# Optimization experiments

Hardware: AMD Instinct MI355X
Metric: run time of the kernel (lower is better)

Reference implementation:

```python
import jax, jax.numpy as jnp
import numpy as np

T, B, I, H, C, O = 4096, 8, 256, 512, 1024, 512
SCHEDULE = 1.0
UPPER_T = 0.3
NIND = int((1.0 - SCHEDULE) * (C - 2) * UPPER_T) + 1  # = 1 (argmax WTA)


def setup_inputs() -> dict:
    key = jax.random.key(0)
    ks = jax.random.split(key, 8)
    def lin(k, fan_out, fan_in):
        s = 1.0 / np.sqrt(fan_in)
        kw, kb = jax.random.split(k)
        return (jax.random.uniform(kw, (fan_out, fan_in), jnp.float32, -s, s),
                jax.random.uniform(kb, (fan_out,), jnp.float32, -s, s))
    i2m_w, i2m_b = lin(ks[0], H, I)
    m2h_w, m2h_b = lin(ks[1], C, H)
    h2o_w, h2o_b = lin(ks[2], O, C)
    return {
        "x": jax.random.normal(ks[3], (T, B, I), jnp.float32),
        "hidden1": jnp.zeros((1,), jnp.float32),  # unused dummy (overwritten in torch forward)
        "i2m_w": i2m_w, "i2m_b": i2m_b,
        "m2h_w": m2h_w, "m2h_b": m2h_b,
        "h2o_w": h2o_w, "h2o_b": h2o_b,
    }


def reference(x, hidden1, i2m_w, i2m_b, m2h_w, m2h_b, h2o_w, h2o_b):
    # linear -> relu
    h = jax.nn.relu(jnp.einsum('tbi,hi->tbh', x, i2m_w) + i2m_b)
    # linear -> relu -> concept pre-activations [T,B,C]
    c = jax.nn.relu(jnp.einsum('tbh,ch->tbc', h, m2h_w) + m2h_b)
    # winner-take-all: top-Nind scatter mask (replaces CPU argsort round-trip)
    _, idx = jax.lax.top_k(c, NIND)  # [T,B,NIND]
    t_ix = jnp.arange(c.shape[0])[:, None, None]
    b_ix = jnp.arange(c.shape[1])[None, :, None]
    mask = jnp.zeros_like(c).at[t_ix, b_ix, idx].set(1.0)
    m = c * mask
    # L2 normalize over concept axis
    m = m / jnp.linalg.norm(m, axis=-1, keepdims=True)
    out = jnp.einsum('tbc,oc->tbo', m, h2o_w) + h2o_b
    return jax.nn.log_softmax(out, axis=-1)
```

## Files before the change

kernel.cpp:

```cpp
#include <hip/hip_runtime.h>
#include <stdint.h>

#define M_ROWS 32768
#define I_DIM 256
#define H_DIM 512
#define C_DIM 1024
#define O_DIM 512

typedef __attribute__((ext_vector_type(8))) short bf16x8;
typedef __attribute__((ext_vector_type(4))) float f32x4;

__device__ __forceinline__ ushort bf16_rne(float f) {
    unsigned u = __float_as_uint(f);
    unsigned r = u + 0x7FFFu + ((u >> 16) & 1u);
    return (ushort)(r >> 16);
}
__device__ __forceinline__ float bf16_f32(ushort h) {
    return __uint_as_float(((unsigned)h) << 16);
}
__device__ __forceinline__ void split2(float f, ushort& hi, ushort& mid) {
    hi = bf16_rne(f);
    mid = bf16_rne(f - bf16_f32(hi));
}

__device__ __forceinline__ void async_ld16(const void* g, void* l) {
    __builtin_amdgcn_global_load_lds(
        (const __attribute__((address_space(1))) void*)g,
        (__attribute__((address_space(3))) void*)l, 16, 0, 0);
}

__device__ __forceinline__ unsigned long long packvi(float v, int col) {
    unsigned u = __float_as_uint(v);
    u = (u & 0x80000000u) ? ~u : (u | 0x80000000u);
    return ((unsigned long long)u << 32) | (unsigned)(~col);
}

__device__ __forceinline__ int slot_of(int kc, int row) {
    return (kc + ((row >> 1) & 3)) & 3;
}

__global__ __launch_bounds__(256)
void prep(const float* __restrict__ W1, ushort* __restrict__ w1h, ushort* __restrict__ w1m,
          const float* __restrict__ W2, ushort* __restrict__ w2h, ushort* __restrict__ w2m,
          const float* __restrict__ Wo, const float* __restrict__ bo,
          float* __restrict__ LS, unsigned long long* __restrict__ part) {
    __shared__ float sred[4];
    const int b = blockIdx.x;
    const int t = threadIdx.x;
    if (b < 320) {
        const int isW1 = (b < 64);
        const float* W = isW1 ? W1 : W2;
        ushort* hh = isW1 ? w1h : w2h;
        ushort* mm = isW1 ? w1m : w2m;
        const int K = isW1 ? I_DIM : H_DIM;
        const int cpr = K >> 3;
        int gid = (isW1 ? b : b - 64) * 256 + t;
        int row = gid / cpr;
        int rem = gid - row * cpr;
        int g = rem >> 2, kc = rem & 3;
        float4 v0 = *(const float4*)(W + (size_t)gid * 8);
        float4 v1 = *(const float4*)(W + (size_t)gid * 8 + 4);
        __align__(16) ushort h[8], m[8];
        float f[8];
        *(float4*)&f[0] = v0; *(float4*)&f[4] = v1;
        #pragma unroll
        for (int j = 0; j < 8; ++j) split2(f[j], h[j], m[j]);
        size_t dst = (size_t)row * K + g * 32 + slot_of(kc, row) * 8;
        *(uint4*)(hh + dst) = *(uint4*)h;
        *(uint4*)(mm + dst) = *(uint4*)m;
    } else if (b < 1344) {
        const int j = b - 320;
        float l0 = Wo[(size_t)t * C_DIM + j] + bo[t];
        float l1 = Wo[(size_t)(t + 256) * C_DIM + j] + bo[t + 256];

        float mx = fmaxf(l0, l1);
        #pragma unroll
        for (int off = 1; off < 64; off <<= 1)
            mx = fmaxf(mx, __shfl_xor(mx, off, 64));
        if ((t & 63) == 0) sred[t >> 6] = mx;
        __syncthreads();
        mx = fmaxf(fmaxf(sred[0], sred[1]), fmaxf(sred[2], sred[3]));
        __syncthreads();

        float s = expf(l0 - mx) + expf(l1 - mx);
        #pragma unroll
        for (int off = 1; off < 64; off <<= 1)
            s += __shfl_xor(s, off, 64);
        if ((t & 63) == 0) sred[t >> 6] = s;
        __syncthreads();
        s = sred[0] + sred[1] + sred[2] + sred[3];

        float lse = mx + logf(s);
        LS[(size_t)j * O_DIM + t] = l0 - lse;
        LS[(size_t)j * O_DIM + t + 256] = l1 - lse;
    } else {
        part[(b - 1344) * 256 + t] = 0ull;
    }
}

__global__ __launch_bounds__(512, 2)
void gemm1_mfma(const float* __restrict__ X, const ushort* __restrict__ W1h,
                const ushort* __restrict__ W1m, const float* __restrict__ b1,
                ushort* __restrict__ Hh, ushort* __restrict__ Hm) {
    __shared__ __align__(16) ushort SMEM[65536];

    const int tid = threadIdx.x;
    const int lane = tid & 63, wave = tid >> 6;
    const int wm = wave >> 2, wn = wave & 3;
    const int lcol = lane & 15, quad = lane >> 4;
    const int lrow = lane >> 2, lk = (lane & 3) * 8;

    const int d = blockIdx.x;
    const int q = d >> 3;
    const int mT = ((d & 7) << 4) + (q >> 1);
    const int nT = q & 1;
    const int mBase = mT * 256;
    const int nBase = nT * 256;

    const int s_row = tid >> 1, s_half = tid & 1;
    const int sl0 = slot_of(s_half * 2,     s_row);
    const int sl1 = slot_of(s_half * 2 + 1, s_row);
    const float* xrow = X + (size_t)(mBase + s_row) * I_DIM + s_half * 16;

    const int bplane = wave >> 2;
    const int brow0 = (wave & 3) * 64;
    const ushort* wp = bplane ? W1m : W1h;
    const ushort* gks = wp + (size_t)(nBase + brow0 + lrow) * I_DIM + lk;

    f32x4 acc[8][4];
    #pragma unroll
    for (int i = 0; i < 8; ++i)
        #pragma unroll
        for (int j = 0; j < 4; ++j)
            acc[i][j] = (f32x4){0.f, 0.f, 0.f, 0.f};

    int aoff[8], boff[4];
    #pragma unroll
    for (int t = 0; t < 8; ++t) {
        int ra = wm * 128 + t * 16 + lcol;
        aoff[t] = ra * 32 + slot_of(quad, ra) * 8;
    }
    #pragma unroll
    for (int t = 0; t < 4; ++t) {
        int rb = wn * 64 + t * 16 + lcol;
        boff[t] = rb * 32 + slot_of(quad, rb) * 8;
    }

    auto loadX = [&](float* f, int k0) {
        const float* ap = xrow + k0;
        *(float4*)&f[0]  = ((const float4*)ap)[0];
        *(float4*)&f[4]  = ((const float4*)ap)[1];
        *(float4*)&f[8]  = ((const float4*)ap)[2];
        *(float4*)&f[12] = ((const float4*)ap)[3];
    };
    auto stageB = [&](int buf, int k0) {
        ushort* bb = SMEM + 32768 + buf * 16384 + bplane * 8192 + brow0 * 32;
        #pragma unroll
        for (int j = 0; j < 4; ++j)
            async_ld16(gks + k0 + (size_t)(j * 16) * I_DIM, bb + j * 512);
    };
    auto writeA = [&](int buf, const float* f) {
        ushort* a0 = SMEM + buf * 16384;
        ushort* a1 = a0 + 8192;
        bf16x8 h0, h1, m0, m1;
        #pragma unroll
        for (int j = 0; j < 8; ++j) {
            ushort hu, mu;
            split2(f[j], hu, mu);
            h0[j] = (short)hu; m0[j] = (short)mu;
            split2(f[j + 8], hu, mu);
            h1[j] = (short)hu; m1[j] = (short)mu;
        }
        *(bf16x8*)&a0[s_row * 32 + sl0 * 8] = h0;
        *(bf16x8*)&a0[s_row * 32 + sl1 * 8] = h1;
        *(bf16x8*)&a1[s_row * 32 + sl0 * 8] = m0;
        *(bf16x8*)&a1[s_row * 32 + sl1 * 8] = m1;
    };

    {
        float fx[16];
        loadX(fx, 0);
        stageB(0, 0);
        writeA(0, fx);
    }
    asm volatile("s_waitcnt lgkmcnt(0)" ::: "memory");
    asm volatile("s_waitcnt vmcnt(0)" ::: "memory");
    __builtin_amdgcn_s_barrier();
    __builtin_amdgcn_sched_barrier(0);

    const int NK = I_DIM / 32;
    #pragma unroll 2
    for (int ks = 0; ks < NK; ++ks) {
        const int cur = ks & 1;
        const bool more = (ks + 1 < NK);
        const ushort* Ac0 = SMEM + cur * 16384;
        const ushort* Ac1 = Ac0 + 8192;
        const ushort* Bc0 = SMEM + 32768 + cur * 16384;
        const ushort* Bc1 = Bc0 + 8192;

        float fn[16];
        if (more) {
            loadX(fn, (ks + 1) * 32);
            stageB(cur ^ 1, (ks + 1) * 32);
            __builtin_amdgcn_sched_barrier(0);
        }

        bf16x8 bh[4], bm[4];
        #pragma unroll
        for (int nt = 0; nt < 4; ++nt) {
            bh[nt] = *(const bf16x8*)&Bc0[boff[nt]];
            bm[nt] = *(const bf16x8*)&Bc1[boff[nt]];
        }
        #pragma unroll
        for (int half = 0; half < 2; ++half) {
            bf16x8 ah[4], am[4];
            #pragma unroll
            for (int mt = 0; mt < 4; ++mt) {
                ah[mt] = *(const bf16x8*)&Ac0[aoff[half * 4 + mt]];
                am[mt] = *(const bf16x8*)&Ac1[aoff[half * 4 + mt]];
            }
            __builtin_amdgcn_s_setprio(1);
            #pragma unroll
            for (int nt = 0; nt < 4; ++nt) {
                #pragma unroll
                for (int mt = 0; mt < 4; ++mt) {
                    f32x4 a = acc[half * 4 + mt][nt];
                    a = __builtin_amdgcn_mfma_f32_16x16x32_bf16(am[mt], bh[nt], a, 0, 0, 0);
                    a = __builtin_amdgcn_mfma_f32_16x16x32_bf16(ah[mt], bm[nt], a, 0, 0, 0);
                    a = __builtin_amdgcn_mfma_f32_16x16x32_bf16(ah[mt], bh[nt], a, 0, 0, 0);
                    acc[half * 4 + mt][nt] = a;
                }
            }
            __builtin_amdgcn_s_setprio(0);
        }

        if (more) writeA(cur ^ 1, fn);
        asm volatile("s_waitcnt lgkmcnt(0)" ::: "memory");
        if (more)
            asm volatile("s_waitcnt vmcnt(0)" ::: "memory");
        __builtin_amdgcn_s_barrier();
        __builtin_amdgcn_sched_barrier(0);
    }

    #pragma unroll
    for (int plane = 0; plane < 2; ++plane) {
        __syncthreads();
        #pragma unroll
        for (int nt = 0; nt < 4; ++nt) {
            int colRel = wn * 64 + nt * 16 + lcol;
            int g = colRel >> 5, kc = (colRel >> 3) & 3, pos = colRel & 7;
            float bias = b1[nBase + colRel];
            #pragma unroll
            for (int mt = 0; mt < 8; ++mt) {
                #pragma unroll
                for (int r = 0; r < 4; ++r) {
                    int rowRel = wm * 128 + mt * 16 + quad * 4 + r;
                    float v = fmaxf(acc[mt][nt][r] + bias, 0.f);
                    ushort hu, mu;
                    split2(v, hu, mu);
                    SMEM[rowRel * 256 + g * 32 + slot_of(kc, rowRel) * 8 + pos]
                        = plane ? mu : hu;
                }
            }
        }
        __syncthreads();
        ushort* dstp = plane ? Hm : Hh;
        #pragma unroll
        for (int l2 = 0; l2 < 16; ++l2) {
            int c = l2 * 512 + tid;
            int row = c >> 5, idx = c & 31;
            *(uint4*)(dstp + (size_t)(mBase + row) * H_DIM + nBase + idx * 8)
                = *(const uint4*)&SMEM[row * 256 + idx * 8];
        }
    }
}

__global__ __launch_bounds__(512, 2)
void gemm2_mfma(const ushort* __restrict__ Hh, const ushort* __restrict__ Hm,
                const ushort* __restrict__ W2h, const ushort* __restrict__ W2m,
                const float* __restrict__ b2,
                unsigned long long* __restrict__ part) {
    __shared__ __align__(16) ushort As[2][2][8192];
    __shared__ __align__(16) ushort Bs[2][2][8192];
    const int tid = threadIdx.x;
    const int lane = tid & 63, wave = tid >> 6;
    const int wm = wave >> 2, wn = wave & 3;
    const int lcol = lane & 15, quad = lane >> 4;
    const int lrow = lane >> 2, lk = (lane & 3) * 8;

    const int d = blockIdx.x;
    const int l = d >> 3;
    const int mT = ((d & 7) << 4) + (l >> 2);
    const int nT = l & 3;
    const int mBase = mT * 256;
    const int nBase = nT * 256;

    const int m_id = wave >> 1;
    const int shalf = wave & 1;
    const ushort* gsrc;
    ushort* l0;
    ushort* l1;
    switch (m_id) {
        case 0:  gsrc = Hh  + (size_t)mBase * H_DIM; l0 = &As[0][0][0]; l1 = &As[1][0][0]; break;
        case 1:  gsrc = Hm  + (size_t)mBase * H_DIM; l0 = &As[0][1][0]; l1 = &As[1][1][0]; break;
        case 2:  gsrc = W2h + (size_t)nBase * H_DIM; l0 = &Bs[0][0][0]; l1 = &Bs[1][0][0]; break;
        default: gsrc = W2m + (size_t)nBase * H_DIM; l0 = &Bs[0][1][0]; l1 = &Bs[1][1][0]; break;
    }
    l0 += shalf * 4096;
    l1 += shalf * 4096;
    const ushort* gks = gsrc + (size_t)(shalf * 128 + lrow) * H_DIM + lk;

    f32x4 acc[8][4];
    #pragma unroll
    for (int i = 0; i < 8; ++i)
        #pragma unroll
        for (int j = 0; j < 4; ++j)
            acc[i][j] = (f32x4){0.f, 0.f, 0.f, 0.f};

    int aoff[8], boff[4];
    #pragma unroll
    for (int t = 0; t < 8; ++t) {
        int ra = wm * 128 + t * 16 + lcol;
        aoff[t] = ra * 32 + slot_of(quad, ra) * 8;
    }
    #pragma unroll
    for (int t = 0; t < 4; ++t) {
        int rb = wn * 64 + t * 16 + lcol;
        boff[t] = rb * 32 + slot_of(quad, rb) * 8;
    }

    auto stage = [&](ushort* lb, int k0) {
        #pragma unroll
        for (int j = 0; j < 8; ++j)
            async_ld16(gks + k0 + (size_t)(j * 16) * H_DIM, lb + j * 512);
    };

    stage(l0, 0);
    asm volatile("s_waitcnt vmcnt(0)" ::: "memory");
    __builtin_amdgcn_s_barrier();
    __builtin_amdgcn_sched_barrier(0);

    const int NK = H_DIM / 32;
    #pragma unroll 2
    for (int ks = 0; ks < NK; ++ks) {
        const int cur = ks & 1;
        if (ks < NK - 1) {
            stage(cur ? l0 : l1, (ks + 1) * 32);
            __builtin_amdgcn_sched_barrier(0);
        }

        bf16x8 bh[4], bm[4];
        #pragma unroll
        for (int nt = 0; nt < 4; ++nt) {
            bh[nt] = *(const bf16x8*)&Bs[cur][0][boff[nt]];
            bm[nt] = *(const bf16x8*)&Bs[cur][1][boff[nt]];
        }
        #pragma unroll
        for (int half = 0; half < 2; ++half) {
            bf16x8 ah[4], am[4];
            #pragma unroll
            for (int mt = 0; mt < 4; ++mt) {
                ah[mt] = *(const bf16x8*)&As[cur][0][aoff[half * 4 + mt]];
                am[mt] = *(const bf16x8*)&As[cur][1][aoff[half * 4 + mt]];
            }
            __builtin_amdgcn_s_setprio(1);
            #pragma unroll
            for (int nt = 0; nt < 4; ++nt) {
                #pragma unroll
                for (int mt = 0; mt < 4; ++mt) {
                    f32x4 a = acc[half * 4 + mt][nt];
                    a = __builtin_amdgcn_mfma_f32_16x16x32_bf16(am[mt], bh[nt], a, 0, 0, 0);
                    a = __builtin_amdgcn_mfma_f32_16x16x32_bf16(ah[mt], bm[nt], a, 0, 0, 0);
                    a = __builtin_amdgcn_mfma_f32_16x16x32_bf16(ah[mt], bh[nt], a, 0, 0, 0);
                    acc[half * 4 + mt][nt] = a;
                }
            }
            __builtin_amdgcn_s_setprio(0);
        }

        if (ks < NK - 1)
            asm volatile("s_waitcnt vmcnt(0)" ::: "memory");
        __builtin_amdgcn_s_barrier();
        __builtin_amdgcn_sched_barrier(0);
    }

    float bias[4];
    #pragma unroll
    for (int nt = 0; nt < 4; ++nt)
        bias[nt] = b2[nBase + wn * 64 + nt * 16 + lcol];

    #pragma unroll
    for (int mt = 0; mt < 8; ++mt) {
        #pragma unroll
        for (int r = 0; r < 4; ++r) {
            unsigned long long best = 0ull;
            #pragma unroll
            for (int nt = 0; nt < 4; ++nt) {
                int col = nBase + wn * 64 + nt * 16 + lcol;
                float v = acc[mt][nt][r] + bias[nt];
                unsigned long long p = packvi(v, col);
                if (p > best) best = p;
            }
            #pragma unroll
            for (int off = 1; off < 16; off <<= 1) {
                unsigned long long o = __shfl_xor((long long)best, off, 64);
                if (o > best) best = o;
            }
            if (lcol == 0) {
                int row = mBase + wm * 128 + mt * 16 + quad * 4 + r;
                atomicMax(&part[row], best);
            }
        }
    }
}

__global__ __launch_bounds__(256)
void gather_out(const unsigned long long* __restrict__ part,
                const float* __restrict__ LS, float* __restrict__ out) {
    __shared__ int js[8];
    const int tid = threadIdx.x;
    const int rbase = blockIdx.x * 8;
    if (tid < 8) {
        unsigned long long best = part[rbase + tid];
        unsigned u = (unsigned)(best >> 32);
        float v = (u & 0x80000000u) ? __uint_as_float(u ^ 0x80000000u)
                                    : __uint_as_float(~u);
        int col = (int)(~(unsigned)best) & (C_DIM - 1);
        js[tid] = (v > 0.f) ? col : 0;
    }
    __syncthreads();
    const float4* LS4 = (const float4*)LS;
    float4* out4 = (float4*)out + (size_t)rbase * 128;
    #pragma unroll
    for (int i = 0; i < 4; ++i) {
        int idx = i * 256 + tid;
        int row = idx >> 7, q = idx & 127;
        out4[idx] = LS4[(size_t)js[row] * 128 + q];
    }
}

extern "C" void kernel_launch(void* const* d_in, const int* in_sizes, int n_in,
                              void* d_out, int out_size, void* d_ws, size_t ws_size,
                              hipStream_t stream) {
    const float* x     = (const float*)d_in[0];
    const float* i2m_w = (const float*)d_in[2];
    const float* i2m_b = (const float*)d_in[3];
    const float* m2h_w = (const float*)d_in[4];
    const float* m2h_b = (const float*)d_in[5];
    const float* h2o_w = (const float*)d_in[6];
    const float* h2o_b = (const float*)d_in[7];
    float* out = (float*)d_out;

    char* ws = (char*)d_ws;
    ushort* w1h = (ushort*)(ws);
    ushort* w1m = (ushort*)(ws + 262144);
    ushort* w2h = (ushort*)(ws + 524288);
    ushort* w2m = (ushort*)(ws + 1572864);
    float*  LS  = (float*)(ws + 2621440);
    unsigned long long* part = (unsigned long long*)(ws + 4718592);

    ushort* Hh = (ushort*)d_out;
    ushort* Hm = Hh + (size_t)M_ROWS * H_DIM;

    prep<<<1472, 256, 0, stream>>>(i2m_w, w1h, w1m, m2h_w, w2h, w2m,
                                   h2o_w, h2o_b, LS, part);
    gemm1_mfma<<<(M_ROWS / 256) * (H_DIM / 256), 512, 0, stream>>>(
        x, w1h, w1m, i2m_b, Hh, Hm);
    gemm2_mfma<<<(M_ROWS / 256) * (C_DIM / 256), 512, 0, stream>>>(
        Hh, Hm, w2h, w2m, m2h_b, part);
    gather_out<<<M_ROWS / 8, 256, 0, stream>>>(part, LS, out);
}
```

Before: 240.3 us.

## Fuse all four stages into one persistent kernel with grid barriers

Replaces the prep, gemm1, gemm2 and gather launches with a single 256-block persistent kernel. The stages are separated by software grid barriers built on global atomic counters. This removes the per-launch overhead and the idle tails between kernels. In exchange it relies on all 256 blocks being co-resident, and a timeout guard in the spin loop could let a block pass the barrier early. Gemm2 now runs its 512 tiles over 256 blocks, and each block handles a larger gather chunk.

Result: slower. 307.8 us (+28.1%).

```diff
diff --git a/kernel.cpp b/kernel.cpp
--- a/kernel.cpp
+++ b/kernel.cpp
@@ -10,6 +10,8 @@
 typedef __attribute__((ext_vector_type(8))) short bf16x8;
 typedef __attribute__((ext_vector_type(4))) float f32x4;
 
+__device__ unsigned g_bar[4] = {0u, 0u, 0u, 0u};
+
 __device__ __forceinline__ ushort bf16_rne(float f) {
     unsigned u = __float_as_uint(f);
     unsigned r = u + 0x7FFFu + ((u >> 16) & 1u);
@@ -39,403 +41,427 @@
     return (kc + ((row >> 1) & 3)) & 3;
 }
 
-__global__ __launch_bounds__(256)
-void prep(const float* __restrict__ W1, ushort* __restrict__ w1h, ushort* __restrict__ w1m,
-          const float* __restrict__ W2, ushort* __restrict__ w2h, ushort* __restrict__ w2m,
-          const float* __restrict__ Wo, const float* __restrict__ bo,
-          float* __restrict__ LS, unsigned long long* __restrict__ part) {
-    __shared__ float sred[4];
+__device__ __forceinline__ void grid_sync(int s) {
+    __syncthreads();
+    if (threadIdx.x == 0) {
+        __threadfence();
+        unsigned old = atomicAdd(&g_bar[s], 1u);
+        unsigned target = (old & ~255u) + 256u;
+        unsigned long long guard = 0ull;
+        while (atomicAdd(&g_bar[s], 0u) < target) {
+            __builtin_amdgcn_s_sleep(2);
+            if (++guard > 10000000ull) break;
+        }
+        __threadfence();
+    }
+    __syncthreads();
+}
+
+__global__ __launch_bounds__(512, 2)
+void mega(const float* X, const float* W1, const float* b1,
+          const float* W2, const float* b2,
+          const float* Wo, const float* bo,
+          ushort* __restrict__ w1h, ushort* __restrict__ w1m,
+          ushort* __restrict__ w2h, ushort* __restrict__ w2m,
+          float* __restrict__ LS, unsigned long long* __restrict__ part,
+          ushort* Hh, ushort* Hm, float* out) {
+    __shared__ __align__(16) ushort SMEM[65536];
+
+    const int tid = threadIdx.x;
     const int b = blockIdx.x;
-    const int t = threadIdx.x;
-    if (b < 320) {
-        const int isW1 = (b < 64);
-        const float* W = isW1 ? W1 : W2;
-        ushort* hh = isW1 ? w1h : w2h;
-        ushort* mm = isW1 ? w1m : w2m;
-        const int K = isW1 ? I_DIM : H_DIM;
-        const int cpr = K >> 3;
-        int gid = (isW1 ? b : b - 64) * 256 + t;
-        int row = gid / cpr;
-        int rem = gid - row * cpr;
-        int g = rem >> 2, kc = rem & 3;
-        float4 v0 = *(const float4*)(W + (size_t)gid * 8);
-        float4 v1 = *(const float4*)(W + (size_t)gid * 8 + 4);
-        __align__(16) ushort h[8], m[8];
-        float f[8];
-        *(float4*)&f[0] = v0; *(float4*)&f[4] = v1;
-        #pragma unroll
-        for (int j = 0; j < 8; ++j) split2(f[j], h[j], m[j]);
-        size_t dst = (size_t)row * K + g * 32 + slot_of(kc, row) * 8;
-        *(uint4*)(hh + dst) = *(uint4*)h;
-        *(uint4*)(mm + dst) = *(uint4*)m;
-    } else if (b < 1344) {
-        const int j = b - 320;
-        float l0 = Wo[(size_t)t * C_DIM + j] + bo[t];
-        float l1 = Wo[(size_t)(t + 256) * C_DIM + j] + bo[t + 256];
-
-        float mx = fmaxf(l0, l1);
-        #pragma unroll
-        for (int off = 1; off < 64; off <<= 1)
-            mx = fmaxf(mx, __shfl_xor(mx, off, 64));
-        if ((t & 63) == 0) sred[t >> 6] = mx;
-        __syncthreads();
-        mx = fmaxf(fmaxf(sred[0], sred[1]), fmaxf(sred[2], sred[3]));
-        __syncthreads();
-
-        float s = expf(l0 - mx) + expf(l1 - mx);
-        #pragma unroll
-        for (int off = 1; off < 64; off <<= 1)
-            s += __shfl_xor(s, off, 64);
-        if ((t & 63) == 0) sred[t >> 6] = s;
-        __syncthreads();
-        s = sred[0] + sred[1] + sred[2] + sred[3];
-
-        float lse = mx + logf(s);
-        LS[(size_t)j * O_DIM + t] = l0 - lse;
-        LS[(size_t)j * O_DIM + t + 256] = l1 - lse;
-    } else {
-        part[(b - 1344) * 256 + t] = 0ull;
-    }
-}
-
-__global__ __launch_bounds__(512, 2)
-void gemm1_mfma(const float* __restrict__ X, const ushort* __restrict__ W1h,
-                const ushort* __restrict__ W1m, const float* __restrict__ b1,
-                ushort* __restrict__ Hh, ushort* __restrict__ Hm) {
-    __shared__ __align__(16) ushort SMEM[65536];
-
-    const int tid = threadIdx.x;
     const int lane = tid & 63, wave = tid >> 6;
     const int wm = wave >> 2, wn = wave & 3;
     const int lcol = lane & 15, quad = lane >> 4;
     const int lrow = lane >> 2, lk = (lane & 3) * 8;
 
-    const int d = blockIdx.x;
-    const int q = d >> 3;
-    const int mT = ((d & 7) << 4) + (q >> 1);
-    const int nT = q & 1;
-    const int mBase = mT * 256;
-    const int nBase = nT * 256;
-
-    const int s_row = tid >> 1, s_half = tid & 1;
-    const int sl0 = slot_of(s_half * 2,     s_row);
-    const int sl1 = slot_of(s_half * 2 + 1, s_row);
-    const float* xrow = X + (size_t)(mBase + s_row) * I_DIM + s_half * 16;
-
-    const int bplane = wave >> 2;
-    const int brow0 = (wave & 3) * 64;
-    const ushort* wp = bplane ? W1m : W1h;
-    const ushort* gks = wp + (size_t)(nBase + brow0 + lrow) * I_DIM + lk;
-
-    f32x4 acc[8][4];
-    #pragma unroll
-    for (int i = 0; i < 8; ++i)
-        #pragma unroll
-        for (int j = 0; j < 4; ++j)
-            acc[i][j] = (f32x4){0.f, 0.f, 0.f, 0.f};
-
-    int aoff[8], boff[4];
-    #pragma unroll
-    for (int t = 0; t < 8; ++t) {
-        int ra = wm * 128 + t * 16 + lcol;
-        aoff[t] = ra * 32 + slot_of(quad, ra) * 8;
+    {
+        int gid = b * 512 + tid;
+        if (gid < 81920) {
+            const int isW1 = (gid < 16384);
+            const float* W = isW1 ? W1 : W2;
+            ushort* hh = isW1 ? w1h : w2h;
+            ushort* mm = isW1 ? w1m : w2m;
+            const int K = isW1 ? I_DIM : H_DIM;
+            const int cpr = K >> 3;
+            int cid = isW1 ? gid : gid - 16384;
+            int row = cid / cpr;
+            int rem = cid - row * cpr;
+            int g = rem >> 2, kc = rem & 3;
+            float4 v0 = *(const float4*)(W + (size_t)cid * 8);
+            float4 v1 = *(const float4*)(W + (size_t)cid * 8 + 4);
+            __align__(16) ushort h[8], m[8];
+            float f[8];
+            *(float4*)&f[0] = v0; *(float4*)&f[4] = v1;
+            #pragma unroll
+            for (int j = 0; j < 8; ++j) split2(f[j], h[j], m[j]);
+            size_t dst = (size_t)row * K + g * 32 + slot_of(kc, row) * 8;
+            *(uint4*)(hh + dst) = *(uint4*)h;
+            *(uint4*)(mm + dst) = *(uint4*)m;
+        }
+        if (gid < 32768) part[gid] = 0ull;
+        float* sred = (float*)SMEM;
+        #pragma unroll 1
+        for (int jj = 0; jj < 4; ++jj) {
+            const int j = b * 4 + jj;
+            float l0 = 0.f, l1 = 0.f, mx = 0.f;
+            if (tid < 256) {
+                l0 = Wo[(size_t)tid * C_DIM + j] + bo[tid];
+                l1 = Wo[(size_t)(tid + 256) * C_DIM + j] + bo[tid + 256];
+                mx = fmaxf(l0, l1);
+                #pragma unroll
+                for (int off = 1; off < 64; off <<= 1)
+                    mx = fmaxf(mx, __shfl_xor(mx, off, 64));
+                if ((tid & 63) == 0) sred[tid >> 6] = mx;
+            }
+            __syncthreads();
+            mx = fmaxf(fmaxf(sred[0], sred[1]), fmaxf(sred[2], sred[3]));
+            __syncthreads();
+            float s = 0.f;
+            if (tid < 256) {
+                s = expf(l0 - mx) + expf(l1 - mx);
+                #pragma unroll
+                for (int off = 1; off < 64; off <<= 1)
+                    s += __shfl_xor(s, off, 64);
+                if ((tid & 63) == 0) sred[tid >> 6] = s;
+            }
+            __syncthreads();
+            s = sred[0] + sred[1] + sred[2] + sred[3];
+            if (tid < 256) {
+                float lse = mx + logf(s);
+                LS[(size_t)j * O_DIM + tid] = l0 - lse;
+                LS[(size_t)j * O_DIM + tid + 256] = l1 - lse;
+            }
+            __syncthreads();
+        }
     }
-    #pragma unroll
-    for (int t = 0; t < 4; ++t) {
-        int rb = wn * 64 + t * 16 + lcol;
-        boff[t] = rb * 32 + slot_of(quad, rb) * 8;
-    }
-
-    auto loadX = [&](float* f, int k0) {
-        const float* ap = xrow + k0;
-        *(float4*)&f[0]  = ((const float4*)ap)[0];
-        *(float4*)&f[4]  = ((const float4*)ap)[1];
-        *(float4*)&f[8]  = ((const float4*)ap)[2];
-        *(float4*)&f[12] = ((const float4*)ap)[3];
-    };
-    auto stageB = [&](int buf, int k0) {
-        ushort* bb = SMEM + 32768 + buf * 16384 + bplane * 8192 + brow0 * 32;
-        #pragma unroll
-        for (int j = 0; j < 4; ++j)
-            async_ld16(gks + k0 + (size_t)(j * 16) * I_DIM, bb + j * 512);
-    };
-    auto writeA = [&](int buf, const float* f) {
-        ushort* a0 = SMEM + buf * 16384;
-        ushort* a1 = a0 + 8192;
-        bf16x8 h0, h1, m0, m1;
-        #pragma unroll
-        for (int j = 0; j < 8; ++j) {
-            ushort hu, mu;
-            split2(f[j], hu, mu);
-            h0[j] = (short)hu; m0[j] = (short)mu;
-            split2(f[j + 8], hu, mu);
-            h1[j] = (short)hu; m1[j] = (short)mu;
-        }
-        *(bf16x8*)&a0[s_row * 32 + sl0 * 8] = h0;
-        *(bf16x8*)&a0[s_row * 32 + sl1 * 8] = h1;
-        *(bf16x8*)&a1[s_row * 32 + sl0 * 8] = m0;
-        *(bf16x8*)&a1[s_row * 32 + sl1 * 8] = m1;
-    };
+    grid_sync(0);
 
     {
-        float fx[16];
-        loadX(fx, 0);
-        stageB(0, 0);
-        writeA(0, fx);
-    }
-    asm volatile("s_waitcnt lgkmcnt(0)" ::: "memory");
-    asm volatile("s_waitcnt vmcnt(0)" ::: "memory");
-    __builtin_amdgcn_s_barrier();
-    __builtin_amdgcn_sched_barrier(0);
-
-    const int NK = I_DIM / 32;
-    #pragma unroll 2
-    for (int ks = 0; ks < NK; ++ks) {
-        const int cur = ks & 1;
-        const bool more = (ks + 1 < NK);
-        const ushort* Ac0 = SMEM + cur * 16384;
-        const ushort* Ac1 = Ac0 + 8192;
-        const ushort* Bc0 = SMEM + 32768 + cur * 16384;
-        const ushort* Bc1 = Bc0 + 8192;
-
-        float fn[16];
-        if (more) {
-            loadX(fn, (ks + 1) * 32);
-            stageB(cur ^ 1, (ks + 1) * 32);
-            __builtin_amdgcn_sched_barrier(0);
-        }
-
-        bf16x8 bh[4], bm[4];
-        #pragma unroll
-        for (int nt = 0; nt < 4; ++nt) {
-            bh[nt] = *(const bf16x8*)&Bc0[boff[nt]];
-            bm[nt] = *(const bf16x8*)&Bc1[boff[nt]];
-        }
-        #pragma unroll
-        for (int half = 0; half < 2; ++half) {
-            bf16x8 ah[4], am[4];
-            #pragma unroll
-            for (int mt = 0; mt < 4; ++mt) {
-                ah[mt] = *(const bf16x8*)&Ac0[aoff[half * 4 + mt]];
-                am[mt] = *(const bf16x8*)&Ac1[aoff[half * 4 + mt]];
-            }
-            __builtin_amdgcn_s_setprio(1);
-            #pragma unroll
-            for (int nt = 0; nt < 4; ++nt) {
-                #pragma unroll
-                for (int mt = 0; mt < 4; ++mt) {
-                    f32x4 a = acc[half * 4 + mt][nt];
-                    a = __builtin_amdgcn_mfma_f32_16x16x32_bf16(am[mt], bh[nt], a, 0, 0, 0);
-                    a = __builtin_amdgcn_mfma_f32_16x16x32_bf16(ah[mt], bm[nt], a, 0, 0, 0);
-                    a = __builtin_amdgcn_mfma_f32_16x16x32_bf16(ah[mt], bh[nt], a, 0, 0, 0);
-                    acc[half * 4 + mt][nt] = a;
-                }
-            }
-            __builtin_amdgcn_s_setprio(0);
-        }
-
-        if (more) writeA(cur ^ 1, fn);
+        const int d = b;
+        const int q = d >> 3;
+        const int mT = ((d & 7) << 4) + (q >> 1);
+        const int nT = q & 1;
+        const int mBase = mT * 256;
+        const int nBase = nT * 256;
+
+        const int s_row = tid >> 1, s_half = tid & 1;
+        const int sl0 = slot_of(s_half * 2,     s_row);
+        const int sl1 = slot_of(s_half * 2 + 1, s_row);
+        const float* xrow = X + (size_t)(mBase + s_row) * I_DIM + s_half * 16;
+
+        const int bplane = wave >> 2;
+        const int brow0 = (wave & 3) * 64;
+        const ushort* wp = bplane ? w1m : w1h;
+        const ushort* gks = wp + (size_t)(nBase + brow0 + lrow) * I_DIM + lk;
+
+        f32x4 acc[8][4];
+        #pragma unroll
+        for (int i = 0; i < 8; ++i)
+            #pragma unroll
+            for (int j = 0; j < 4; ++j)
+                acc[i][j] = (f32x4){0.f, 0.f, 0.f, 0.f};
+
+        int aoff[8], boff[4];
+        #pragma unroll
+        for (int t = 0; t < 8; ++t) {
+            int ra = wm * 128 + t * 16 + lcol;
+            aoff[t] = ra * 32 + slot_of(quad, ra) * 8;
+        }
+        #pragma unroll
+        for (int t = 0; t < 4; ++t) {
+            int rb = wn * 64 + t * 16 + lcol;
+            boff[t] = rb * 32 + slot_of(quad, rb) * 8;
+        }
+
+        auto loadX = [&](float* f, int k0) {
+            const float* ap = xrow + k0;
+            *(float4*)&f[0]  = ((const float4*)ap)[0];
+            *(float4*)&f[4]  = ((const float4*)ap)[1];
+            *(float4*)&f[8]  = ((const float4*)ap)[2];
+            *(float4*)&f[12] = ((const float4*)ap)[3];
+        };
+        auto stageB = [&](int buf, int k0) {
+            ushort* bb = SMEM + 32768 + buf * 16384 + bplane * 8192 + brow0 * 32;
+            #pragma unroll
+            for (int j = 0; j < 4; ++j)
+                async_ld16(gks + k0 + (size_t)(j * 16) * I_DIM, bb + j * 512);
+        };
+        auto writeA = [&](int buf, const float* f) {
+            ushort* a0 = SMEM + buf * 16384;
+            ushort* a1 = a0 + 8192;
+            bf16x8 h0, h1, m0, m1;
+            #pragma unroll
+            for (int j = 0; j < 8; ++j) {
+                ushort hu, mu;
+                split2(f[j], hu, mu);
+                h0[j] = (short)hu; m0[j] = (short)mu;
+                split2(f[j + 8], hu, mu);
+                h1[j] = (short)hu; m1[j] = (short)mu;
+            }
+            *(bf16x8*)&a0[s_row * 32 + sl0 * 8] = h0;
+            *(bf16x8*)&a0[s_row * 32 + sl1 * 8] = h1;
+            *(bf16x8*)&a1[s_row * 32 + sl0 * 8] = m0;
+            *(bf16x8*)&a1[s_row * 32 + sl1 * 8] = m1;
+        };
+
+        {
+            float fx[16];
+            loadX(fx, 0);
+            stageB(0, 0);
+            writeA(0, fx);
+        }
         asm volatile("s_waitcnt lgkmcnt(0)" ::: "memory");
-        if (more)
-            asm volatile("s_waitcnt vmcnt(0)" ::: "memory");
+        asm volatile("s_waitcnt vmcnt(0)" ::: "memory");
         __builtin_amdgcn_s_barrier();
         __builtin_amdgcn_sched_barrier(0);
+
+        const int NK = I_DIM / 32;
+        #pragma unroll 2
+        for (int ks = 0; ks < NK; ++ks) {
+            const int cur = ks & 1;
+            const bool more = (ks + 1 < NK);
+            const ushort* Ac0 = SMEM + cur * 16384;
+            const ushort* Ac1 = Ac0 + 8192;
+            const ushort* Bc0 = SMEM + 32768 + cur * 16384;
+            const ushort* Bc1 = Bc0 + 8192;
+
+            float fn[16];
+            if (more) {
+                loadX(fn, (ks + 1) * 32);
+                stageB(cur ^ 1, (ks + 1) * 32);
+                __builtin_amdgcn_sched_barrier(0);
+            }
+
+            bf16x8 bh[4], bm[4];
+            #pragma unroll
+            for (int nt = 0; nt < 4; ++nt) {
+                bh[nt] = *(const bf16x8*)&Bc0[boff[nt]];
+                bm[nt] = *(const bf16x8*)&Bc1[boff[nt]];
+            }
+            #pragma unroll
+            for (int half = 0; half < 2; ++half) {
+                bf16x8 ah[4], am[4];
+                #pragma unroll
+                for (int mt = 0; mt < 4; ++mt) {
+                    ah[mt] = *(const bf16x8*)&Ac0[aoff[half * 4 + mt]];
+                    am[mt] = *(const bf16x8*)&Ac1[aoff[half * 4 + mt]];
+                }
+                __builtin_amdgcn_s_setprio(1);
+                #pragma unroll
+                for (int nt = 0; nt < 4; ++nt) {
+                    #pragma unroll
+                    for (int mt = 0; mt < 4; ++mt) {
+                        f32x4 a = acc[half * 4 + mt][nt];
+                        a = __builtin_amdgcn_mfma_f32_16x16x32_bf16(am[mt], bh[nt], a, 0, 0, 0);
+                        a = __builtin_amdgcn_mfma_f32_16x16x32_bf16(ah[mt], bm[nt], a, 0, 0, 0);
+                        a = __builtin_amdgcn_mfma_f32_16x16x32_bf16(ah[mt], bh[nt], a, 0, 0, 0);
+                        acc[half * 4 + mt][nt] = a;
+                    }
+                }
+                __builtin_amdgcn_s_setprio(0);
+            }
+
+            if (more) writeA(cur ^ 1, fn);
+            asm volatile("s_waitcnt lgkmcnt(0)" ::: "memory");
+            if (more)
+                asm volatile("s_waitcnt vmcnt(0)" ::: "memory");
+            __builtin_amdgcn_s_barrier();
+            __builtin_amdgcn_sched_barrier(0);
+        }
+
+        #pragma unroll
+        for (int plane = 0; plane < 2; ++plane) {
+            __syncthreads();
+            #pragma unroll
+            for (int nt = 0; nt < 4; ++nt) {
+                int colRel = wn * 64 + nt * 16 + lcol;
+                int g = colRel >> 5, kc = (colRel >> 3) & 3, pos = colRel & 7;
+                float bias = b1[nBase + colRel];
+                #pragma unroll
+                for (int mt = 0; mt < 8; ++mt) {
+                    #pragma unroll
+                    for (int r = 0; r < 4; ++r) {
+                        int rowRel = wm * 128 + mt * 16 + quad * 4 + r;
+                        float v = fmaxf(acc[mt][nt][r] + bias, 0.f);
+                        ushort hu, mu;
+                        split2(v, hu, mu);
+                        SMEM[rowRel * 256 + g * 32 + slot_of(kc, rowRel) * 8 + pos]
+                            = plane ? mu : hu;
+                    }
+                }
+            }
+            __syncthreads();
+            ushort* dstp = plane ? Hm : Hh;
+            #pragma unroll
+            for (int l2 = 0; l2 < 16; ++l2) {
+                int c = l2 * 512 + tid;
+                int row = c >> 5, idx = c & 31;
+                *(uint4*)(dstp + (size_t)(mBase + row) * H_DIM + nBase + idx * 8)
+                    = *(const uint4*)&SMEM[row * 256 + idx * 8];
+            }
+        }
     }
-
-    #pragma unroll
-    for (int plane = 0; plane < 2; ++plane) {
+    grid_sync(1);
+
+    {
+        ushort* As_base = SMEM;
+        ushort* Bs_base = SMEM + 32768;
+
+        int aoff[8], boff[4];
+        #pragma unroll
+        for (int t = 0; t < 8; ++t) {
+            int ra = wm * 128 + t * 16 + lcol;
+            aoff[t] = ra * 32 + slot_of(quad, ra) * 8;
+        }
+        #pragma unroll
+        for (int t = 0; t < 4; ++t) {
+            int rb = wn * 64 + t * 16 + lcol;
+            boff[t] = rb * 32 + slot_of(quad, rb) * 8;
+        }
+
+        const int m_id = wave >> 1;
+        const int shalf = wave & 1;
+
+        #pragma unroll 1
+        for (int rnd = 0; rnd < 2; ++rnd) {
+            const int d = b + rnd * 256;
+            const int l = d >> 3;
+            const int mT = ((d & 7) << 4) + (l >> 2);
+            const int nT = l & 3;
+            const int mBase = mT * 256;
+            const int nBase = nT * 256;
+
+            const ushort* gsrc;
+            ushort* lbase;
+            switch (m_id) {
+                case 0:  gsrc = Hh  + (size_t)mBase * H_DIM; lbase = As_base;        break;
+                case 1:  gsrc = Hm  + (size_t)mBase * H_DIM; lbase = As_base + 8192; break;
+                case 2:  gsrc = w2h + (size_t)nBase * H_DIM; lbase = Bs_base;        break;
+                default: gsrc = w2m + (size_t)nBase * H_DIM; lbase = Bs_base + 8192; break;
+            }
+            ushort* l0 = lbase + shalf * 4096;
+            ushort* l1 = lbase + 16384 + shalf * 4096;
+            const ushort* gks = gsrc + (size_t)(shalf * 128 + lrow) * H_DIM + lk;
+
+            f32x4 acc[8][4];
+            #pragma unroll
+            for (int i = 0; i < 8; ++i)
+                #pragma unroll
+                for (int j = 0; j < 4; ++j)
+                    acc[i][j] = (f32x4){0.f, 0.f, 0.f, 0.f};
+
+            auto stage = [&](ushort* lb, int k0) {
+                #pragma unroll
+                for (int j = 0; j < 8; ++j)
+                    async_ld16(gks + k0 + (size_t)(j * 16) * H_DIM, lb + j * 512);
+            };
+
+            __syncthreads();
+            stage(l0, 0);
+            asm volatile("s_waitcnt vmcnt(0)" ::: "memory");
+            __builtin_amdgcn_s_barrier();
+            __builtin_amdgcn_sched_barrier(0);
+
+            const int NK = H_DIM / 32;
+            #pragma unroll 2
+            for (int ks = 0; ks < NK; ++ks) {
+                const int cur = ks & 1;
+                if (ks < NK - 1) {
+                    stage(cur ? l0 : l1, (ks + 1) * 32);
+                    __builtin_amdgcn_sched_barrier(0);
+                }
+                const ushort* Ac0 = As_base + cur * 16384;
+                const ushort* Ac1 = Ac0 + 8192;
+                const ushort* Bc0 = Bs_base + cur * 16384;
+                const ushort* Bc1 = Bc0 + 8192;
+
+                bf16x8 bh[4], bm[4];
+                #pragma unroll
+                for (int nt = 0; nt < 4; ++nt) {
+                    bh[nt] = *(const bf16x8*)&Bc0[boff[nt]];
+                    bm[nt] = *(const bf16x8*)&Bc1[boff[nt]];
+                }
+                #pragma unroll
+                for (int half = 0; half < 2; ++half) {
+                    bf16x8 ah[4], am[4];
+                    #pragma unroll
+                    for (int mt = 0; mt < 4; ++mt) {
+                        ah[mt] = *(const bf16x8*)&Ac0[aoff[half * 4 + mt]];
+                        am[mt] = *(const bf16x8*)&Ac1[aoff[half * 4 + mt]];
+                    }
+                    __builtin_amdgcn_s_setprio(1);
+                    #pragma unroll
+                    for (int nt = 0; nt < 4; ++nt) {
+                        #pragma unroll
+                        for (int mt = 0; mt < 4; ++mt) {
+                            f32x4 a = acc[half * 4 + mt][nt];
+                            a = __builtin_amdgcn_mfma_f32_16x16x32_bf16(am[mt], bh[nt], a, 0, 0, 0);
+                            a = __builtin_amdgcn_mfma_f32_16x16x32_bf16(ah[mt], bm[nt], a, 0, 0, 0);
+                            a = __builtin_amdgcn_mfma_f32_16x16x32_bf16(ah[mt], bh[nt], a, 0, 0, 0);
+                            acc[half * 4 + mt][nt] = a;
+                        }
+                    }
+                    __builtin_amdgcn_s_setprio(0);
+                }
+
+                if (ks < NK - 1)
+                    asm volatile("s_waitcnt vmcnt(0)" ::: "memory");
+                __builtin_amdgcn_s_barrier();
+                __builtin_amdgcn_sched_barrier(0);
+            }
+
+            float bias[4];
+            #pragma unroll
+            for (int nt = 0; nt < 4; ++nt)
+                bias[nt] = b2[nBase + wn * 64 + nt * 16 + lcol];
+
+            #pragma unroll
+            for (int mt = 0; mt < 8; ++mt) {
+                #pragma unroll
+                for (int r = 0; r < 4; ++r) {
+                    unsigned long long best = 0ull;
+                    #pragma unroll
+                    for (int nt = 0; nt < 4; ++nt) {
+                        int col = nBase + wn * 64 + nt * 16 + lcol;
+                        float v = acc[mt][nt][r] + bias[nt];
+                        unsigned long long p = packvi(v, col);
+                        if (p > best) best = p;
+                    }
+                    #pragma unroll
+                    for (int off = 1; off < 16; off <<= 1) {
+                        unsigned long long o = __shfl_xor((long long)best, off, 64);
+                        if (o > best) best = o;
+                    }
+                    if (lcol == 0) {
+                        int row = mBase + wm * 128 + mt * 16 + quad * 4 + r;
+                        atomicMax(&part[row], best);
+                    }
+                }
+            }
+        }
+    }
+    grid_sync(2);
+
+    {
+        int* js = (int*)SMEM;
+        const int rbase = b * 128;
+        if (tid < 128) {
+            unsigned long long best = atomicAdd(&part[rbase + tid], 0ull);
+            unsigned u = (unsigned)(best >> 32);
+            float v = (u & 0x80000000u) ? __uint_as_float(u ^ 0x80000000u)
+                                        : __uint_as_float(~u);
+            int col = (int)(~(unsigned)best) & (C_DIM - 1);
+            js[tid] = (v > 0.f) ? col : 0;
+        }
         __syncthreads();
-        #pragma unroll
-        for (int nt = 0; nt < 4; ++nt) {
-            int colRel = wn * 64 + nt * 16 + lcol;
-            int g = colRel >> 5, kc = (colRel >> 3) & 3, pos = colRel & 7;
-            float bias = b1[nBase + colRel];
-            #pragma unroll
-            for (int mt = 0; mt < 8; ++mt) {
-                #pragma unroll
-                for (int r = 0; r < 4; ++r) {
-                    int rowRel = wm * 128 + mt * 16 + quad * 4 + r;
-                    float v = fmaxf(acc[mt][nt][r] + bias, 0.f);
-                    ushort hu, mu;
-                    split2(v, hu, mu);
-                    SMEM[rowRel * 256 + g * 32 + slot_of(kc, rowRel) * 8 + pos]
-                        = plane ? mu : hu;
-                }
-            }
-        }
-        __syncthreads();
-        ushort* dstp = plane ? Hm : Hh;
-        #pragma unroll
-        for (int l2 = 0; l2 < 16; ++l2) {
-            int c = l2 * 512 + tid;
-            int row = c >> 5, idx = c & 31;
-            *(uint4*)(dstp + (size_t)(mBase + row) * H_DIM + nBase + idx * 8)
-                = *(const uint4*)&SMEM[row * 256 + idx * 8];
-        }
-    }
-}
-
-__global__ __launch_bounds__(512, 2)
-void gemm2_mfma(const ushort* __restrict__ Hh, const ushort* __restrict__ Hm,
-                const ushort* __restrict__ W2h, const ushort* __restrict__ W2m,
-                const float* __restrict__ b2,
-                unsigned long long* __restrict__ part) {
-    __shared__ __align__(16) ushort As[2][2][8192];
-    __shared__ __align__(16) ushort Bs[2][2][8192];
-    const int tid = threadIdx.x;
-    const int lane = tid & 63, wave = tid >> 6;
-    const int wm = wave >> 2, wn = wave & 3;
-    const int lcol = lane & 15, quad = lane >> 4;
-    const int lrow = lane >> 2, lk = (lane & 3) * 8;
-
-    const int d = blockIdx.x;
-    const int l = d >> 3;
-    const int mT = ((d & 7) << 4) + (l >> 2);
-    const int nT = l & 3;
-    const int mBase = mT * 256;
-    const int nBase = nT * 256;
-
-    const int m_id = wave >> 1;
-    const int shalf = wave & 1;
-    const ushort* gsrc;
-    ushort* l0;
-    ushort* l1;
-    switch (m_id) {
-        case 0:  gsrc = Hh  + (size_t)mBase * H_DIM; l0 = &As[0][0][0]; l1 = &As[1][0][0]; break;
-        case 1:  gsrc = Hm  + (size_t)mBase * H_DIM; l0 = &As[0][1][0]; l1 = &As[1][1][0]; break;
-        case 2:  gsrc = W2h + (size_t)nBase * H_DIM; l0 = &Bs[0][0][0]; l1 = &Bs[1][0][0]; break;
-        default: gsrc = W2m + (size_t)nBase * H_DIM; l0 = &Bs[0][1][0]; l1 = &Bs[1][1][0]; break;
-    }
-    l0 += shalf * 4096;
-    l1 += shalf * 4096;
-    const ushort* gks = gsrc + (size_t)(shalf * 128 + lrow) * H_DIM + lk;
-
-    f32x4 acc[8][4];
-    #pragma unroll
-    for (int i = 0; i < 8; ++i)
-        #pragma unroll
-        for (int j = 0; j < 4; ++j)
-            acc[i][j] = (f32x4){0.f, 0.f, 0.f, 0.f};
-
-    int aoff[8], boff[4];
-    #pragma unroll
-    for (int t = 0; t < 8; ++t) {
-        int ra = wm * 128 + t * 16 + lcol;
-        aoff[t] = ra * 32 + slot_of(quad, ra) * 8;
-    }
-    #pragma unroll
-    for (int t = 0; t < 4; ++t) {
-        int rb = wn * 64 + t * 16 + lcol;
-        boff[t] = rb * 32 + slot_of(quad, rb) * 8;
-    }
-
-    auto stage = [&](ushort* lb, int k0) {
-        #pragma unroll
-        for (int j = 0; j < 8; ++j)
-            async_ld16(gks + k0 + (size_t)(j * 16) * H_DIM, lb + j * 512);
-    };
-
-    stage(l0, 0);
-    asm volatile("s_waitcnt vmcnt(0)" ::: "memory");
-    __builtin_amdgcn_s_barrier();
-    __builtin_amdgcn_sched_barrier(0);
-
-    const int NK = H_DIM / 32;
-    #pragma unroll 2
-    for (int ks = 0; ks < NK; ++ks) {
-        const int cur = ks & 1;
-        if (ks < NK - 1) {
-            stage(cur ? l0 : l1, (ks + 1) * 32);
-            __builtin_amdgcn_sched_barrier(0);
-        }
-
-        bf16x8 bh[4], bm[4];
-        #pragma unroll
-        for (int nt = 0; nt < 4; ++nt) {
-            bh[nt] = *(const bf16x8*)&Bs[cur][0][boff[nt]];
-            bm[nt] = *(const bf16x8*)&Bs[cur][1][boff[nt]];
-        }
-        #pragma unroll
-        for (int half = 0; half < 2; ++half) {
-            bf16x8 ah[4], am[4];
-            #pragma unroll
-            for (int mt = 0; mt < 4; ++mt) {
-                ah[mt] = *(const bf16x8*)&As[cur][0][aoff[half * 4 + mt]];
-                am[mt] = *(const bf16x8*)&As[cur][1][aoff[half * 4 + mt]];
-            }
-            __builtin_amdgcn_s_setprio(1);
-            #pragma unroll
-            for (int nt = 0; nt < 4; ++nt) {
-                #pragma unroll
-                for (int mt = 0; mt < 4; ++mt) {
-                    f32x4 a = acc[half * 4 + mt][nt];
-                    a = __builtin_amdgcn_mfma_f32_16x16x32_bf16(am[mt], bh[nt], a, 0, 0, 0);
-                    a = __builtin_amdgcn_mfma_f32_16x16x32_bf16(ah[mt], bm[nt], a, 0, 0, 0);
-                    a = __builtin_amdgcn_mfma_f32_16x16x32_bf16(ah[mt], bh[nt], a, 0, 0, 0);
-                    acc[half * 4 + mt][nt] = a;
-                }
-            }
-            __builtin_amdgcn_s_setprio(0);
-        }
-
-        if (ks < NK - 1)
-            asm volatile("s_waitcnt vmcnt(0)" ::: "memory");
-        __builtin_amdgcn_s_barrier();
-        __builtin_amdgcn_sched_barrier(0);
-    }
-
-    float bias[4];
-    #pragma unroll
-    for (int nt = 0; nt < 4; ++nt)
-        bias[nt] = b2[nBase + wn * 64 + nt * 16 + lcol];
-
-    #pragma unroll
-    for (int mt = 0; mt < 8; ++mt) {
-        #pragma unroll
-        for (int r = 0; r < 4; ++r) {
-            unsigned long long best = 0ull;
-            #pragma unroll
-            for (int nt = 0; nt < 4; ++nt) {
-                int col = nBase + wn * 64 + nt * 16 + lcol;
-                float v = acc[mt][nt][r] + bias[nt];
-                unsigned long long p = packvi(v, col);
-                if (p > best) best = p;
-            }
-            #pragma unroll
-            for (int off = 1; off < 16; off <<= 1) {
-                unsigned long long o = __shfl_xor((long long)best, off, 64);
-                if (o > best) best = o;
-            }
-            if (lcol == 0) {
-                int row = mBase + wm * 128 + mt * 16 + quad * 4 + r;
-                atomicMax(&part[row], best);
-            }
-        }
-    }
-}
-
-__global__ __launch_bounds__(256)
-void gather_out(const unsigned long long* __restrict__ part,
-                const float* __restrict__ LS, float* __restrict__ out) {
-    __shared__ int js[8];
-    const int tid = threadIdx.x;
-    const int rbase = blockIdx.x * 8;
-    if (tid < 8) {
-        unsigned long long best = part[rbase + tid];
-        unsigned u = (unsigned)(best >> 32);
-        float v = (u & 0x80000000u) ? __uint_as_float(u ^ 0x80000000u)
-                                    : __uint_as_float(~u);
-        int col = (int)(~(unsigned)best) & (C_DIM - 1);
-        js[tid] = (v > 0.f) ? col : 0;
-    }
-    __syncthreads();
-    const float4* LS4 = (const float4*)LS;
-    float4* out4 = (float4*)out + (size_t)rbase * 128;
-    #pragma unroll
-    for (int i = 0; i < 4; ++i) {
-        int idx = i * 256 + tid;
-        int row = idx >> 7, q = idx & 127;
-        out4[idx] = LS4[(size_t)js[row] * 128 + q];
+        const float4* LS4 = (const float4*)LS;
+        float4* out4 = (float4*)out + (size_t)rbase * 128;
+        #pragma unroll
+        for (int i = 0; i < 32; ++i) {
+            int idx = i * 512 + tid;
+            int row = idx >> 7, q = idx & 127;
+            out4[idx] = LS4[(size_t)js[row] * 128 + q];
+        }
     }
 }
 
@@ -462,11 +488,8 @@
     ushort* Hh = (ushort*)d_out;
     ushort* Hm = Hh + (size_t)M_ROWS * H_DIM;
 
-    prep<<<1472, 256, 0, stream>>>(i2m_w, w1h, w1m, m2h_w, w2h, w2m,
-                                   h2o_w, h2o_b, LS, part);
-    gemm1_mfma<<<(M_ROWS / 256) * (H_DIM / 256), 512, 0, stream>>>(
-        x, w1h, w1m, i2m_b, Hh, Hm);
-    gemm2_mfma<<<(M_ROWS / 256) * (C_DIM / 256), 512, 0, stream>>>(
-        Hh, Hm, w2h, w2m, m2h_b, part);
-    gather_out<<<M_ROWS / 8, 256, 0, stream>>>(part, LS, out);
-}
+    mega<<<256, 512, 0, stream>>>(x, i2m_w, i2m_b, m2h_w, m2h_b,
+                                  h2o_w, h2o_b,
+                                  w1h, w1m, w2h, w2m, LS, part,
+                                  Hh, Hm, out);
+}
```
